# Optimization experiments

Measured on AMD Instinct MI355X. Metric: run time of the kernel, lower is better.

Reference implementation:

```python
import jax, jax.numpy as jnp
import numpy as np
import math

N, S, R = 1, 128, 256
CM, CZ, C, MSA_H, PAIR_H, CTM, FF = 256, 128, 32, 8, 4, 128, 4
SCALE = 1.0 / math.sqrt(C)


def _ln(x, w, b):
    m = jnp.mean(x, -1, keepdims=True)
    v = jnp.var(x, -1, keepdims=True)
    return (x - m) / jnp.sqrt(v + 1e-5) * w + b


def _gated_attn(x, gate_w, qkv_w, out_w, head, bias=None):
    # x: [n, s, r, cin]; attention over r within each (n, s, head)
    n, s, r, _ = x.shape
    gate = jax.nn.sigmoid(x @ gate_w).reshape(n, s, r, head, C)
    qkv = (x @ qkv_w).reshape(n, s, r, 3, head, C)
    q, k, v = qkv[..., 0, :, :], qkv[..., 1, :, :], qkv[..., 2, :, :]
    sim = jax.nn.softmax(jnp.einsum('nsqhc,nskhc->nshqk', q, k) * SCALE, axis=-1)
    if bias is not None:
        sim = sim + bias  # NOTE: source adds bias AFTER softmax; kept faithful
    att = jnp.einsum('nshqk,nskhc->nsqhc', sim, v) * gate
    return att.reshape(n, s, r, head * C) @ out_w


def _tri_mul(x, n1w, n1b, n2w, n2b, p1, p2, p3, p4, p5, p6, incoming):
    xn = _ln(x, n1w, n1b)
    a = jax.nn.sigmoid(xn @ p1) * (xn @ p2)
    b = jax.nn.sigmoid(xn @ p3) * (xn @ p4)
    if incoming:
        p = jnp.einsum('nrsk,nrtk->nstk', a, b)
        g = jnp.swapaxes(jax.nn.sigmoid(xn @ p6), 1, 2)
    else:
        p = jnp.einsum('nsrk,ntrk->nstk', a, b)
        g = jax.nn.sigmoid(xn @ p6)
    return (_ln(p, n2w, n2b) @ p5) * g


def setup_inputs() -> dict:
    keys = iter(jax.random.split(jax.random.key(0), 80))

    def rn(shape, scale=0.02):
        return jax.random.normal(next(keys), shape, dtype=jnp.float32) * scale

    ones = lambda n: jnp.ones((n,), jnp.float32)
    zeros = lambda n: jnp.zeros((n,), jnp.float32)
    d = dict(
        msa_repr=rn((N, S, R, CM), 1.0),
        pair_repr=rn((N, R, R, CZ), 1.0),
        row_norm_m_w=ones(CM), row_norm_m_b=zeros(CM),
        row_norm_z_w=ones(CZ), row_norm_z_b=zeros(CZ),
        row_gate=rn((CM, MSA_H * C)), row_qkv=rn((CM, 3 * MSA_H * C)),
        row_out=rn((MSA_H * C, CM)), row_bias=rn((CZ, MSA_H)),
        col_norm_w=ones(CM), col_norm_b=zeros(CM),
        col_gate=rn((CM, MSA_H * C)), col_qkv=rn((CM, 3 * MSA_H * C)),
        col_out=rn((MSA_H * C, CM)),
        mt_norm_w=ones(CM), mt_norm_b=zeros(CM),
        mt_p1=rn((CM, FF * CM)), mt_p2=rn((FF * CM, CM)),
        outer_norm_w=ones(CM), outer_norm_b=zeros(CM),
        outer_p1=rn((CM, C)), outer_p2=rn((CM, C)), outer_out=rn((C * C, CZ)),
        tmo_n1_w=ones(CZ), tmo_n1_b=zeros(CZ), tmo_n2_w=ones(CTM), tmo_n2_b=zeros(CTM),
        tmo_p1=rn((CZ, CTM)), tmo_p2=rn((CZ, CTM)), tmo_p3=rn((CZ, CTM)), tmo_p4=rn((CZ, CTM)),
        tmo_p5=rn((CTM, CZ)), tmo_p6=rn((CZ, CZ)),
        tmi_n1_w=ones(CZ), tmi_n1_b=zeros(CZ), tmi_n2_w=ones(CTM), tmi_n2_b=zeros(CTM),
        tmi_p1=rn((CZ, CTM)), tmi_p2=rn((CZ, CTM)), tmi_p3=rn((CZ, CTM)), tmi_p4=rn((CZ, CTM)),
        tmi_p5=rn((CTM, CZ)), tmi_p6=rn((CZ, CZ)),
        tas_norm_w=ones(CZ), tas_norm_b=zeros(CZ),
        tas_gate=rn((CZ, PAIR_H * C)), tas_qkv=rn((CZ, 3 * PAIR_H * C)),
        tas_out=rn((PAIR_H * C, CZ)), tas_bias=rn((CZ, PAIR_H)),
        tae_norm_w=ones(CZ), tae_norm_b=zeros(CZ),
        tae_gate=rn((CZ, PAIR_H * C)), tae_qkv=rn((CZ, 3 * PAIR_H * C)),
        tae_out=rn((PAIR_H * C, CZ)), tae_bias=rn((CZ, PAIR_H)),
        pt_norm_w=ones(CZ), pt_norm_b=zeros(CZ),
        pt_p1=rn((CZ, FF * CZ)), pt_p2=rn((FF * CZ, CZ)),
    )
    return d


def reference(msa_repr, pair_repr, row_norm_m_w, row_norm_m_b, row_norm_z_w, row_norm_z_b, row_gate, row_qkv, row_out, row_bias, col_norm_w, col_norm_b, col_gate, col_qkv, col_out, mt_norm_w, mt_norm_b, mt_p1, mt_p2, outer_norm_w, outer_norm_b, outer_p1, outer_p2, outer_out, tmo_n1_w, tmo_n1_b, tmo_n2_w, tmo_n2_b, tmo_p1, tmo_p2, tmo_p3, tmo_p4, tmo_p5, tmo_p6, tmi_n1_w, tmi_n1_b, tmi_n2_w, tmi_n2_b, tmi_p1, tmi_p2, tmi_p3, tmi_p4, tmi_p5, tmi_p6, tas_norm_w, tas_norm_b, tas_gate, tas_qkv, tas_out, tas_bias, tae_norm_w, tae_norm_b, tae_gate, tae_qkv, tae_out, tae_bias, pt_norm_w, pt_norm_b, pt_p1, pt_p2):
    msa, pair = msa_repr, pair_repr
    # 1. MSA row attention with pair bias
    xm = _ln(msa, row_norm_m_w, row_norm_m_b)
    xz = _ln(pair, row_norm_z_w, row_norm_z_b)
    bias = jnp.transpose(xz @ row_bias, (0, 3, 1, 2))[:, None]  # [N,1,H,R,R]
    msa = msa + _gated_attn(xm, row_gate, row_qkv, row_out, MSA_H, bias)
    # 2. MSA column attention
    xm = _ln(msa, col_norm_w, col_norm_b)
    msa = msa + jnp.swapaxes(_gated_attn(jnp.swapaxes(xm, 1, 2), col_gate, col_qkv, col_out, MSA_H), 1, 2)
    # 3. MSA transition
    xm = _ln(msa, mt_norm_w, mt_norm_b)
    msa = msa + jax.nn.relu(xm @ mt_p1) @ mt_p2
    # 4. outer product mean (no division in source; sum over s)
    xm = _ln(msa, outer_norm_w, outer_norm_b)
    a = jnp.swapaxes(xm @ outer_p1, 1, 2)  # [n,r,s,c]
    b = jnp.swapaxes(xm @ outer_p2, 1, 2)  # [n,t,s,c]
    outer = jnp.einsum('nrsc,ntse->nrtce', a, b).reshape(a.shape[0], a.shape[1], b.shape[1], C * C)
    pair = pair + outer @ outer_out
    # 5/6. triangle multiplicative updates (outgoing then incoming)
    pair = pair + _tri_mul(pair, tmo_n1_w, tmo_n1_b, tmo_n2_w, tmo_n2_b, tmo_p1, tmo_p2, tmo_p3, tmo_p4, tmo_p5, tmo_p6, False)
    pair = pair + _tri_mul(pair, tmi_n1_w, tmi_n1_b, tmi_n2_w, tmi_n2_b, tmi_p1, tmi_p2, tmi_p3, tmi_p4, tmi_p5, tmi_p6, True)
    # 7. triangle attention (node start)
    xz = _ln(pair, tas_norm_w, tas_norm_b)
    bias = jnp.transpose(xz @ tas_bias, (0, 1, 3, 2))[:, :, :, None, :]  # [N,S,H,1,R]
    pair = pair + _gated_attn(xz, tas_gate, tas_qkv, tas_out, PAIR_H, bias)
    # 8. triangle attention (node end): transpose residue axes
    xz = jnp.swapaxes(_ln(pair, tae_norm_w, tae_norm_b), 1, 2)
    bias = jnp.transpose(xz @ tae_bias, (0, 1, 3, 2))[:, :, :, None, :]
    pair = pair + jnp.swapaxes(_gated_attn(xz, tae_gate, tae_qkv, tae_out, PAIR_H, bias), 1, 2)
    # 9. pair transition
    xz = _ln(pair, pt_norm_w, pt_norm_b)
    pair = pair + jax.nn.relu(xz @ pt_p1) @ pt_p2
    return msa, pair
```

## Files before the change

### kernel.cpp

```cpp
#include <hip/hip_runtime.h>
#include <hip/hip_bf16.h>
#include <stdint.h>

typedef __hip_bfloat16 bf16;
typedef __attribute__((ext_vector_type(4))) int   i32x4;
typedef __attribute__((ext_vector_type(2))) unsigned u32x2;
typedef __attribute__((ext_vector_type(4))) float f32x4;


__device__ __forceinline__ float toF(float x){ return x; }
__device__ __forceinline__ float toF(bf16 x){ return __bfloat162float(x); }
__device__ __forceinline__ bf16  toB(float x){ return __float2bfloat16(x); }

__device__ __forceinline__ void gload16(const bf16* g, bf16* l){
    __builtin_amdgcn_global_load_lds((const __attribute__((address_space(1))) void*)g,
                                     (__attribute__((address_space(3))) void*)l, 16, 0, 0);
}

#define NW_IN 58
struct WStage {
    const void* src[NW_IN];
    int off[NW_IN];
    int K[NW_IN], N[NW_IN];
};
__global__ __launch_bounds__(256) void cvt_all_k(WStage t, bf16* __restrict__ base,
                                                 const uint32_t* __restrict__ probe){
    bool isbf = (probe[0] == 0x3F803F80u);
    const int wi = blockIdx.y;
    const void* in = t.src[wi];
    bf16* out = base + t.off[wi];
    const int K = t.K[wi], N = t.N[wi];
    const int total = K ? K*N : N;
    for (int i = blockIdx.x*256 + threadIdx.x; i < total; i += gridDim.x*256){
        float v = isbf ? toF(((const bf16*)in)[i]) : ((const float*)in)[i];
        if (K){ int k = i / N, n = i - k*N; out[(size_t)n*K + k] = toB(v); }
        else    out[i] = toB(v);
    }
}
__global__ void in2f_k(const void* __restrict__ in, float* __restrict__ out, int n,
                       const uint32_t* __restrict__ probe){
    bool isbf = (probe[0] == 0x3F803F80u);
    int i = blockIdx.x*256 + threadIdx.x;
    if (i < n) out[i] = isbf ? toF(((const bf16*)in)[i]) : ((const float*)in)[i];
}

template<typename T>
__global__ void ln_k(const T* __restrict__ x, const bf16* __restrict__ w, const bf16* __restrict__ b,
                     bf16* __restrict__ out, int D){
    int row = blockIdx.x, c = threadIdx.x;
    float v = toF(x[(size_t)row*D + c]);
    float s1 = v, s2 = v*v;
    #pragma unroll
    for (int o=32;o>0;o>>=1){ s1 += __shfl_down(s1,o); s2 += __shfl_down(s2,o); }
    __shared__ float r1[4], r2[4];
    int lane = c & 63, wid = c >> 6;
    if (lane==0){ r1[wid]=s1; r2[wid]=s2; }
    __syncthreads();
    int nw = blockDim.x >> 6;
    float m=0.f, q=0.f;
    for (int i=0;i<nw;i++){ m+=r1[i]; q+=r2[i]; }
    m /= (float)D; q = q/(float)D - m*m;
    float inv = rsqrtf(q + 1e-5f);
    out[(size_t)row*D + c] = toB((v-m)*inv*toF(w[c]) + toF(b[c]));
}

template<int MODE, int HN>
__global__ __launch_bounds__(256) void bproj_k(const bf16* __restrict__ xz, const bf16* __restrict__ Wb,
                                               bf16* __restrict__ outb){
    __shared__ float WbS[128*HN];
    const int i = blockIdx.x, t = threadIdx.x;
    for (int idx = t; idx < 128*HN; idx += 256) WbS[idx] = toF(Wb[idx]);
    __syncthreads();
    const bf16* row = xz + ((size_t)i*256 + t)*128;
    float d[HN] = {};
    #pragma unroll 4
    for (int c8 = 0; c8 < 16; ++c8){
        uint4 v = *(const uint4*)(row + c8*8);
        bf16 tmp[8]; *(uint4*)tmp = v;
        #pragma unroll
        for (int u=0;u<8;u++){
            float x = toF(tmp[u]);
            #pragma unroll
            for (int h=0;h<HN;h++) d[h] += x * WbS[(c8*8+u)*HN + h];
        }
    }
    #pragma unroll
    for (int h=0;h<HN;h++){
        size_t idx = (MODE==0) ? ((size_t)h*65536 + (size_t)i*256 + t)
                   : (MODE==1) ? ((size_t)(i*HN+h)*256 + t)
                               : ((size_t)(t*HN+h)*256 + i);
        outb[idx] = toB(d[h]);
    }
}

template<int ACT, int MUL, int RES, int HM>
__global__ __launch_bounds__(256) void mgemm_k(const bf16* __restrict__ A, const bf16* __restrict__ Bt,
                                               bf16* __restrict__ C, float* __restrict__ Res,
                                               const bf16* __restrict__ Mul,
                                               int M, int N, int K, int lda, size_t astep,
                                               int ldbt, size_t ldc, int res_off, int gtrans){
    __shared__ alignas(16) bf16 As[128*32];
    __shared__ alignas(16) bf16 Bs[128*32];
    const int tid  = threadIdx.x;
    const int m0   = blockIdx.y << 7, n0 = blockIdx.x << 7;
    const int lane = tid & 63, w = tid >> 6;
    const int wr   = (w >> 1) << 6, wc = (w & 1) << 6;
    const int fr   = lane & 15, fq = lane >> 4;
    const int sr = tid >> 2, sc = (tid & 3) << 3;
    const bf16* ga = A  + (size_t)(m0 + sr)*lda  + sc;
    const bf16* gb = Bt + (size_t)(n0 + sr)*ldbt + sc;
    bf16* la = As + tid*8;
    bf16* lb = Bs + tid*8;
    const size_t gaS = (size_t)64*lda, gbS = (size_t)64*ldbt;

    f32x4 acc[4][4] = {};
    for (int k0=0; k0<K; k0+=32){
        gload16(ga, la);        gload16(ga + gaS, la + 2048);
        gload16(gb, lb);        gload16(gb + gbS, lb + 2048);
        ga += astep; gb += 32;
        __syncthreads();
        i32x4 af[4], bv[4];
        #pragma unroll
        for (int i=0;i<4;i++) af[i] = *(const i32x4*)(As + ((wr + i*16 + fr) << 5) + (fq << 3));
        #pragma unroll
        for (int j=0;j<4;j++) bv[j] = *(const i32x4*)(Bs + ((wc + j*16 + fr) << 5) + (fq << 3));
        #pragma unroll
        for (int i=0;i<4;i++)
            #pragma unroll
            for (int j=0;j<4;j++)
                asm("v_mfma_f32_16x16x32_bf16 %0, %1, %2, %0"
                    : "+v"(acc[i][j]) : "v"(af[i]), "v"(bv[j]));
        __syncthreads();
    }
    #pragma unroll
    for (int i=0;i<4;i++){
        const int mB = m0 + wr + i*16 + (fq << 2);
        #pragma unroll
        for (int j=0;j<4;j++){
            const int n = n0 + wc + j*16 + fr;
            #pragma unroll
            for (int r=0;r<4;r++){
                int m = mB + r;
                float x = acc[i][j][r];
                if (ACT==1) x = 1.f/(1.f + __expf(-x));
                else if (ACT==2) x = fmaxf(x, 0.f);
                if (MUL){
                    int mr = gtrans ? (((m & 255) << 8) | (m >> 8)) : m;
                    x *= toF(Mul[(size_t)mr*N + n]);
                }
                if (RES) Res[(size_t)(m + res_off)*N + n] += x;
                else if (HM) C[(size_t)(n>>5)*ldc + (size_t)m*32 + (n&31)] = toB(x);
                else     C[(size_t)m*ldc + n] = toB(x);
            }
        }
    }
}

template<int ACT, int MUL, int RES, int GATE, int MHM>
__global__ __launch_bounds__(256) void sgemm_k(const bf16* __restrict__ A,
        const bf16* __restrict__ Bt1, const bf16* __restrict__ Bt2,
        bf16* __restrict__ C, float* __restrict__ Res, const bf16* __restrict__ Mul,
        int M, int lda, int ldbt, int ldc, size_t ldmul, int res_off, int gtrans){
    __shared__ alignas(16) bf16 Bs1[128*128];
    __shared__ alignas(16) bf16 Bs2[GATE ? 128*128 : 16];
    const int tid = threadIdx.x;
    for (int idx = tid; idx < 2048; idx += 256){
        int n = idx >> 4, cc = idx & 15;
        int sc = (cc ^ (n & 15)) << 3;
        *(uint4*)(Bs1 + n*128 + sc) = *(const uint4*)(Bt1 + (size_t)n*ldbt + (cc<<3));
        if (GATE)
            *(uint4*)(Bs2 + n*128 + sc) = *(const uint4*)(Bt2 + (size_t)n*ldbt + (cc<<3));
    }
    __syncthreads();
    const int lane = tid & 63, w = tid >> 6;
    const int fr = lane & 15, fq = lane >> 4;
    const int mb = blockIdx.x*128 + w*32;
    f32x4 acc[2][8] = {};
    f32x4 acc2[2][8] = {};
    #pragma unroll
    for (int k0=0;k0<4;k0++){
        i32x4 af[2];
        #pragma unroll
        for (int i=0;i<2;i++)
            af[i] = *(const i32x4*)(A + (size_t)(mb + i*16 + fr)*lda + k0*32 + fq*8);
        const int co = ((k0*4 + fq) ^ fr) << 3;
        #pragma unroll
        for (int j=0;j<8;j++){
            i32x4 bf1 = *(const i32x4*)(Bs1 + (j*16+fr)*128 + co);
            #pragma unroll
            for (int i=0;i<2;i++)
                asm("v_mfma_f32_16x16x32_bf16 %0, %1, %2, %0"
                    : "+v"(acc[i][j]) : "v"(af[i]), "v"(bf1));
            if (GATE){
                i32x4 bf2 = *(const i32x4*)(Bs2 + (j*16+fr)*128 + co);
                #pragma unroll
                for (int i=0;i<2;i++)
                    asm("v_mfma_f32_16x16x32_bf16 %0, %1, %2, %0"
                        : "+v"(acc2[i][j]) : "v"(af[i]), "v"(bf2));
            }
        }
    }
    #pragma unroll
    for (int i=0;i<2;i++){
        #pragma unroll
        for (int j=0;j<8;j++){
            const int n = j*16 + fr;
            #pragma unroll
            for (int r=0;r<4;r++){
                int m = mb + i*16 + (fq<<2) + r;
                float x = acc[i][j][r];
                if (GATE) x = acc2[i][j][r] / (1.f + __expf(-x));
                else if (ACT==1) x = 1.f/(1.f + __expf(-x));
                else if (ACT==2) x = fmaxf(x, 0.f);
                if (MUL){
                    int mr = gtrans ? (((m & 255) << 8) | (m >> 8)) : m;
                    if (MHM) x *= toF(Mul[(size_t)(n>>5)*ldmul + (size_t)mr*32 + (n&31)]);
                    else     x *= toF(Mul[(size_t)mr*ldmul + n]);
                }
                if (RES) Res[(size_t)(m + res_off)*128 + n] += x;
                else     C[(size_t)m*ldc + n] = toB(x);
            }
        }
    }
}

__global__ __launch_bounds__(256) void btrimul_k(const bf16* __restrict__ aT, const bf16* __restrict__ bT,
                                                 bf16* __restrict__ pT){
    __shared__ alignas(16) bf16 As[128*32];
    __shared__ alignas(16) bf16 Bs[128*32];
    const int tid  = threadIdx.x;
    const int m0   = blockIdx.y << 7, n0 = blockIdx.x << 7;
    const size_t zb = (size_t)blockIdx.z << 16;
    const int lane = tid & 63, w = tid >> 6;
    const int wr   = (w >> 1) << 6, wc = (w & 1) << 6;
    const int fr   = lane & 15, fq = lane >> 4;
    const int sr = tid >> 2, sc = (tid & 3) << 3;
    const bf16* ga = aT + zb + (size_t)(m0 + sr)*256 + sc;
    const bf16* gb = bT + zb + (size_t)(n0 + sr)*256 + sc;
    bf16* la = As + tid*8;
    bf16* lb = Bs + tid*8;
    const size_t gS = (size_t)64*256;

    f32x4 acc[4][4] = {};
    for (int k0=0; k0<256; k0+=32){
        gload16(ga, la);        gload16(ga + gS, la + 2048);
        gload16(gb, lb);        gload16(gb + gS, lb + 2048);
        ga += 32; gb += 32;
        __syncthreads();
        i32x4 af[4], bv[4];
        #pragma unroll
        for (int i=0;i<4;i++) af[i] = *(const i32x4*)(As + ((wr + i*16 + fr) << 5) + (fq << 3));
        #pragma unroll
        for (int j=0;j<4;j++) bv[j] = *(const i32x4*)(Bs + ((wc + j*16 + fr) << 5) + (fq << 3));
        #pragma unroll
        for (int i=0;i<4;i++)
            #pragma unroll
            for (int j=0;j<4;j++)
                asm("v_mfma_f32_16x16x32_bf16 %0, %1, %2, %0"
                    : "+v"(acc[i][j]) : "v"(af[i]), "v"(bv[j]));
        __syncthreads();
    }
    #pragma unroll
    for (int i=0;i<4;i++){
        const int mB = m0 + wr + i*16 + (fq << 2);
        #pragma unroll
        for (int j=0;j<4;j++){
            const int n = n0 + wc + j*16 + fr;
            #pragma unroll
            for (int r=0;r<4;r++)
                pT[zb + (size_t)(mB + r)*256 + n] = toB(acc[i][j][r]);
        }
    }
}

__global__ __launch_bounds__(256) void rc2k_k(const bf16* __restrict__ in, bf16* __restrict__ out, int swap){
    __shared__ uint16_t T[128][137];
    const int tt = blockIdx.x, tid = threadIdx.x;
    size_t base_pp, out_off; int ppstride;
    if (!swap){ base_pp = (size_t)tt*128;                  ppstride = 1;   out_off = (size_t)tt*128; }
    else      { int J = tt>>1, I0 = (tt&1)*128;
                base_pp = (size_t)I0*256 + J;              ppstride = 256; out_off = (size_t)J*256 + I0; }
    for (int it=0; it<8; ++it){
        int idx = tid + it*256;
        int r = idx >> 4, c8 = (idx & 15) << 3;
        uint4 v = *(const uint4*)(in + (base_pp + (size_t)r*ppstride)*128 + c8);
        uint16_t tmp[8]; *(uint4*)tmp = v;
        #pragma unroll
        for (int t=0;t<8;t++) T[r][c8+t] = tmp[t];
    }
    __syncthreads();
    for (int it=0; it<8; ++it){
        int idx = tid + it*256;
        int k = idx >> 4, r8 = (idx & 15) << 3;
        uint16_t tmp[8];
        #pragma unroll
        for (int t=0;t<8;t++) tmp[t] = T[r8+t][k];
        *(uint4*)(out + (size_t)k*65536 + out_off + r8) = *(uint4*)tmp;
    }
}
__global__ __launch_bounds__(256) void k2rc_k(const bf16* __restrict__ in, bf16* __restrict__ out){
    __shared__ uint16_t T[128][137];
    const int tt = blockIdx.x, tid = threadIdx.x;
    const size_t a0 = (size_t)tt*128;
    for (int it=0; it<8; ++it){
        int idx = tid + it*256;
        int k = idx >> 4, r8 = (idx & 15) << 3;
        uint4 v = *(const uint4*)(in + (size_t)k*65536 + a0 + r8);
        uint16_t tmp[8]; *(uint4*)tmp = v;
        #pragma unroll
        for (int t=0;t<8;t++) T[r8+t][k] = tmp[t];
    }
    __syncthreads();
    for (int it=0; it<8; ++it){
        int idx = tid + it*256;
        int r = idx >> 4, c8 = (idx & 15) << 3;
        uint16_t tmp[8];
        #pragma unroll
        for (int t=0;t<8;t++) tmp[t] = T[r][c8+t];
        *(uint4*)(out + (a0 + r)*128 + c8) = *(uint4*)tmp;
    }
}

template<int ACT, int MUL, int RES>
__global__ __launch_bounds__(256) void gemm_k(const bf16* __restrict__ A, const bf16* __restrict__ Bw,
                                              bf16* __restrict__ C, float* __restrict__ Res,
                                              const bf16* __restrict__ Mul,
                                              int M, int N, int K, int ldb, int res_off, int gtrans){
    __shared__ float As[64][33];
    __shared__ float Bs[32][65];
    int tid = threadIdx.x;
    int m0 = blockIdx.y*64, n0 = blockIdx.x*64;
    int tx = tid & 15, ty = tid >> 4;
    float acc[4][4] = {};
    for (int k0=0; k0<K; k0+=32){
        for (int i=tid; i<64*32; i+=256){
            int r = i>>5, cc = i&31;
            As[r][cc] = toF(A[(size_t)(m0+r)*K + k0 + cc]);
        }
        for (int i=tid; i<32*64; i+=256){
            int r = i>>6, cc = i&63; int col = n0+cc;
            Bs[r][cc] = (col < N) ? toF(Bw[(size_t)(k0+r)*ldb + col]) : 0.f;
        }
        __syncthreads();
        #pragma unroll 8
        for (int k=0;k<32;k++){
            float a4[4], b4[4];
            #pragma unroll
            for (int i=0;i<4;i++) a4[i] = As[ty*4+i][k];
            #pragma unroll
            for (int j=0;j<4;j++) b4[j] = Bs[k][tx*4+j];
            #pragma unroll
            for (int i=0;i<4;i++)
                #pragma unroll
                for (int j=0;j<4;j++) acc[i][j] += a4[i]*b4[j];
        }
        __syncthreads();
    }
    #pragma unroll
    for (int i=0;i<4;i++){
        int m = m0 + ty*4 + i;
        #pragma unroll
        for (int j=0;j<4;j++){
            int n = n0 + tx*4 + j;
            if (n >= N) continue;
            float x = acc[i][j];
            if (ACT==1) x = 1.f/(1.f + __expf(-x));
            else if (ACT==2) x = fmaxf(x, 0.f);
            if (MUL){
                int mr = gtrans ? (((m & 255) << 8) | (m >> 8)) : m;
                x *= toF(Mul[(size_t)mr*N + n]);
            }
            if (RES) Res[(size_t)(m + res_off)*N + n] += x;
            else     C[(size_t)m*N + n] = toB(x);
        }
    }
}

template<int BIAS, int L>
__global__ __launch_bounds__(256) void attn4_k(bf16* __restrict__ QO,
                                               const bf16* __restrict__ Kp, const bf16* __restrict__ Vp,
                                               const bf16* __restrict__ bias,
                                               int H, size_t HS, int sO, int sL){
    constexpr int MW  = L/4;
    constexpr int IFR = MW/16;
    constexpr int KC  = 32;
    constexpr int NCH = L/KC;
    constexpr int VP  = L + 8;
    constexpr int PTW = 44;
    __shared__ alignas(16) bf16 K_lds[L*40];
    __shared__ alignas(16) bf16 VT_lds[32*VP];
    __shared__ alignas(16) bf16 PT_lds[4*MW*PTW];
    __shared__ float red[8*32 + 32];
    const int o = blockIdx.y, h = blockIdx.x, tid = threadIdx.x;
    const int lane = tid & 63, w = tid >> 6;
    const int fr = lane & 15, fq = lane >> 4;
    const size_t hb = (size_t)h*HS;

    for (int idx = tid; idx < L*4; idx += 256){
        int l = idx >> 2, c8 = (idx & 3) << 3;
        size_t p = hb + (size_t)(o*sO + l*sL)*32 + c8;
        *(uint4*)(K_lds + l*40 + c8) = *(const uint4*)(Kp + p);
        uint4 vv = *(const uint4*)(Vp + p);
        bf16 tmp[8]; *(uint4*)tmp = vv;
        #pragma unroll
        for (int t=0;t<8;t++) VT_lds[(c8+t)*VP + l] = tmp[t];
    }
    __syncthreads();

    float* ObS = red + 256;
    if (BIAS == 2){
        int c = tid & 31, g = tid >> 5;
        const bf16* bp = bias + (size_t)(o*H + h)*256;
        float p = 0.f;
        for (int k = g*(L/8); k < (g+1)*(L/8); ++k)
            p += toF(bp[k]) * toF(VT_lds[c*VP + k]);
        red[g*32 + c] = p;
        __syncthreads();
        if (tid < 32){
            float s = 0.f;
            #pragma unroll
            for (int g2=0; g2<8; ++g2) s += red[g2*32 + tid];
            ObS[tid] = s;
        }
        __syncthreads();
    }

    i32x4 qf[IFR];
    #pragma unroll
    for (int i=0;i<IFR;i++){
        int q = w*MW + i*16 + fr;
        qf[i] = *(const i32x4*)(QO + hb + (size_t)(o*sO + q*sL)*32 + fq*8);
    }
    bf16* Pw = PT_lds + w*MW*PTW;
    f32x4 accO[IFR][2] = {};
    f32x4 accB[IFR][2] = {};
    float ls[IFR] = {};

    for (int ch=0; ch<NCH; ++ch){
        const int k0 = ch*KC;
        f32x4 sa[IFR][2] = {};
        i32x4 kf[2];
        #pragma unroll
        for (int j=0;j<2;j++) kf[j] = *(const i32x4*)(K_lds + (k0 + j*16 + fr)*40 + fq*8);
        #pragma unroll
        for (int i=0;i<IFR;i++)
            #pragma unroll
            for (int j=0;j<2;j++)
                asm("v_mfma_f32_16x16x32_bf16 %0, %1, %2, %0"
                    : "+v"(sa[i][j]) : "v"(kf[j]), "v"(qf[i]));
        #pragma unroll
        for (int i=0;i<IFR;i++){
            #pragma unroll
            for (int j=0;j<2;j++){
                float e0 = __expf(sa[i][j][0] * 0.17677669529663687f);
                float e1 = __expf(sa[i][j][1] * 0.17677669529663687f);
                float e2 = __expf(sa[i][j][2] * 0.17677669529663687f);
                float e3 = __expf(sa[i][j][3] * 0.17677669529663687f);
                ls[i] += (e0+e1) + (e2+e3);
                unsigned d0, d1;
                asm("v_cvt_pk_bf16_f32 %0, %1, %2" : "=v"(d0) : "v"(e0), "v"(e1));
                asm("v_cvt_pk_bf16_f32 %0, %1, %2" : "=v"(d1) : "v"(e2), "v"(e3));
                u32x2 dd = {d0, d1};
                *(u32x2*)(Pw + (i*16 + fr)*PTW + j*16 + fq*4) = dd;
            }
        }
        i32x4 vf[2];
        #pragma unroll
        for (int j=0;j<2;j++) vf[j] = *(const i32x4*)(VT_lds + (j*16 + fr)*VP + k0 + fq*8);
        #pragma unroll
        for (int i=0;i<IFR;i++){
            i32x4 pa = *(const i32x4*)(Pw + (i*16 + fr)*PTW + fq*8);
            #pragma unroll
            for (int j=0;j<2;j++)
                asm("v_mfma_f32_16x16x32_bf16 %0, %1, %2, %0"
                    : "+v"(accO[i][j]) : "v"(pa), "v"(vf[j]));
        }
        if (BIAS == 1){
            #pragma unroll
            for (int i=0;i<IFR;i++){
                i32x4 ba = *(const i32x4*)(bias + (size_t)h*65536
                               + (size_t)(w*MW + i*16 + fr)*256 + k0 + fq*8);
                #pragma unroll
                for (int j=0;j<2;j++)
                    asm("v_mfma_f32_16x16x32_bf16 %0, %1, %2, %0"
                        : "+v"(accB[i][j]) : "v"(ba), "v"(vf[j]));
            }
        }
    }
    #pragma unroll
    for (int i=0;i<IFR;i++){
        float s = ls[i];
        s += __shfl_xor(s, 16); s += __shfl_xor(s, 32);
        ls[i] = 1.f / s;
    }
    #pragma unroll
    for (int i=0;i<IFR;i++)
        #pragma unroll
        for (int j=0;j<2;j++)
            #pragma unroll
            for (int r=0;r<4;r++){
                int q = w*MW + i*16 + fq*4 + r;
                int c = j*16 + fr;
                float inv = __shfl(ls[i], fq*4 + r);
                float v = accO[i][j][r]*inv;
                if (BIAS==1) v += accB[i][j][r];
                if (BIAS==2) v += ObS[c];
                QO[hb + (size_t)(o*sO + q*sL)*32 + c] = toB(v);
            }
}

__global__ void mulsigHM_k(bf16* __restrict__ a, const bf16* __restrict__ g, size_t HS, int NC, int n){
    int i = blockIdx.x*256 + threadIdx.x;
    if (i < n){
        int m = i / NC, col = i - m*NC;
        int h = col >> 5, c = col & 31;
        size_t o = (size_t)h*HS + (size_t)m*32 + c;
        float sg = 1.f/(1.f + __expf(-toF(g[(size_t)m*NC + col])));
        a[o] = toB(toF(a[o]) * sg);
    }
}

__global__ __launch_bounds__(256) void outer_k(const bf16* __restrict__ ap, const bf16* __restrict__ bp,
                                               bf16* __restrict__ outc, int r0){
    int t = blockIdx.x, rl = blockIdx.y, r = r0 + rl;
    __shared__ float As[128*32], Bs[128*32];
    for (int idx=threadIdx.x; idx<128*32; idx+=256){
        int s = idx>>5, c = idx&31;
        As[idx] = toF(ap[((size_t)s*256 + r)*32 + c]);
        Bs[idx] = toF(bp[((size_t)s*256 + t)*32 + c]);
    }
    __syncthreads();
    int ce0 = threadIdx.x*4;
    int c = ce0 >> 5, e0 = ce0 & 31;
    float acc[4] = {0.f,0.f,0.f,0.f};
    for (int s=0;s<128;s++){
        float av = As[s*32 + c];
        #pragma unroll
        for (int j=0;j<4;j++) acc[j] += av*Bs[s*32 + e0 + j];
    }
    size_t row = (size_t)rl*256 + t;
    #pragma unroll
    for (int j=0;j<4;j++) outc[row*1024 + ce0 + j] = toB(acc[j]);
}

static bool tshape(int i, int& K, int& N){
    switch(i){
        case 6: case 8: case 12: case 14: K=256; N=256;  return true;
        case 7: case 13:                  K=256; N=768;  return true;
        case 17:                          K=256; N=1024; return true;
        case 18:                          K=1024;N=256;  return true;
        case 23:                          K=1024;N=128;  return true;
        case 47: case 53:                 K=128; N=384;  return true;
        case 58:                          K=128; N=512;  return true;
        case 59:                          K=512; N=128;  return true;
        default:
            if ((i>=28&&i<=33)||(i>=38&&i<=43)||i==46||i==48||i==52||i==54){ K=128; N=128; return true; }
            return false;
    }
}

extern "C" void kernel_launch(void* const* d_in, const int* in_sizes, int n_in,
                              void* d_out, int out_size, void* d_ws, size_t ws_size,
                              hipStream_t stream){
    (void)n_in; (void)out_size; (void)ws_size;
    const int MSA_N  = 128*256*256;
    const int PAIR_N = 256*256*128;
    const size_t HSm = (size_t)32768*32;
    const size_t HSp = (size_t)65536*32;
    const uint32_t* probe = (const uint32_t*)d_in[2];

    char*  w     = (char*)d_ws;
    bf16*  wsts  = (bf16*)(w);
    bf16*  biasB = (bf16*)(w + 4194304);
    bf16*  lnb   = (bf16*)(w + 6291456);
    bf16*  bufA  = (bf16*)(w + 23068672);
    bf16*  bufB  = (bf16*)(w + 39845888);
    bf16*  bufC  = (bf16*)(w + 56623104);

    float* msaF  = (float*)d_out;
    float* pairF = msaF + MSA_N;

    size_t woff[64]; { size_t acc = 0;
        for (int i=2;i<60;i++){ woff[i] = acc; acc += ((size_t)in_sizes[i] + 63) & ~(size_t)63; } }
    #define W(i) (wsts + woff[i])

    {
        WStage st;
        for (int i=2;i<60;i++){
            int tk, tn;
            st.src[i-2] = d_in[i];
            st.off[i-2] = (int)woff[i];
            if (tshape(i, tk, tn)){ st.K[i-2]=tk; st.N[i-2]=tn; }
            else                   { st.K[i-2]=0;  st.N[i-2]=in_sizes[i]; }
        }
        cvt_all_k<<<dim3(64, NW_IN),256,0,stream>>>(st, wsts, probe);
    }

    in2f_k<<<32768,256,0,stream>>>(d_in[0], msaF,  MSA_N,  probe);
    in2f_k<<<32768,256,0,stream>>>(d_in[1], pairF, PAIR_N, probe);

    ln_k<float><<<32768,256,0,stream>>>(msaF, W(2), W(3), lnb, 256);
    ln_k<float><<<65536,128,0,stream>>>(pairF, W(4), W(5), bufC, 128);
    bproj_k<0,8><<<256,256,0,stream>>>(bufC, W(9), biasB);
    mgemm_k<0,0,0,1><<<dim3(6,256),256,0,stream>>>(lnb, W(7), bufA, nullptr, nullptr,
                                                   32768,768,256, 256,32,256, HSm, 0,0);
    attn4_k<1,256><<<dim3(8,128),256,0,stream>>>(bufA, bufA+8*HSm, bufA+16*HSm, biasB, 8, HSm, 256, 1);
    mgemm_k<0,0,0,0><<<dim3(2,256),256,0,stream>>>(lnb, W(6), bufA+8*HSm, nullptr, nullptr,
                                                   32768,256,256, 256,32,256, 256, 0,0);
    mulsigHM_k<<<32768,256,0,stream>>>(bufA, bufA+8*HSm, HSm, 256, MSA_N);
    mgemm_k<0,0,1,0><<<dim3(2,256),256,0,stream>>>(bufA, W(8), nullptr, msaF, nullptr,
                                                   32768,256,256, 32,HSm,256, 256, 0,0);

    ln_k<float><<<32768,256,0,stream>>>(msaF, W(10), W(11), lnb, 256);
    mgemm_k<0,0,0,1><<<dim3(6,256),256,0,stream>>>(lnb, W(13), bufA, nullptr, nullptr,
                                                   32768,768,256, 256,32,256, HSm, 0,0);
    attn4_k<0,128><<<dim3(8,256),256,0,stream>>>(bufA, bufA+8*HSm, bufA+16*HSm, nullptr, 8, HSm, 1, 256);
    mgemm_k<0,0,0,0><<<dim3(2,256),256,0,stream>>>(lnb, W(12), bufA+8*HSm, nullptr, nullptr,
                                                   32768,256,256, 256,32,256, 256, 0,0);
    mulsigHM_k<<<32768,256,0,stream>>>(bufA, bufA+8*HSm, HSm, 256, MSA_N);
    mgemm_k<0,0,1,0><<<dim3(2,256),256,0,stream>>>(bufA, W(14), nullptr, msaF, nullptr,
                                                   32768,256,256, 32,HSm,256, 256, 0,0);

    ln_k<float><<<32768,256,0,stream>>>(msaF, W(15), W(16), lnb, 256);
    for (int ch=0; ch<4; ++ch){
        mgemm_k<2,0,0,0><<<dim3(2,256),256,0,stream>>>(lnb, W(17)+ch*65536, bufA, nullptr, nullptr,
                                                       32768,256,256, 256,32,256, 256, 0,0);
        mgemm_k<0,0,1,0><<<dim3(2,256),256,0,stream>>>(bufA, W(18)+ch*256, nullptr, msaF, nullptr,
                                                       32768,256,256, 256,32,1024, 256, 0,0);
    }

    ln_k<float><<<32768,256,0,stream>>>(msaF, W(19), W(20), lnb, 256);
    gemm_k<0,0,0><<<dim3(1,512),256,0,stream>>>(lnb, W(21), bufA, nullptr, nullptr, 32768,32,256, 32, 0,0);
    gemm_k<0,0,0><<<dim3(1,512),256,0,stream>>>(lnb, W(22), bufB, nullptr, nullptr, 32768,32,256, 32, 0,0);
    for (int ch=0; ch<8; ++ch){
        outer_k<<<dim3(256,32),256,0,stream>>>(bufA, bufB, lnb, ch*32);
        mgemm_k<0,0,1,0><<<dim3(1,64),256,0,stream>>>(lnb, W(23), nullptr, pairF, nullptr,
                                                      8192,128,1024, 1024,32,1024, 128, ch*8192,0);
    }

    for (int tm=0; tm<2; ++tm){
        int o = tm ? 34 : 24;
        int inc = tm;
        ln_k<float><<<65536,128,0,stream>>>(pairF, W(o+0), W(o+1), lnb, 128);
        sgemm_k<0,0,0,1,0><<<512,256,0,stream>>>(lnb, W(o+4), W(o+5), bufA, nullptr, nullptr,
                                                 65536, 128,128,128,0, 0,0);
        sgemm_k<0,0,0,1,0><<<512,256,0,stream>>>(lnb, W(o+6), W(o+7), bufB, nullptr, nullptr,
                                                 65536, 128,128,128,0, 0,0);
        rc2k_k<<<512,256,0,stream>>>(bufA, bufC, inc);
        rc2k_k<<<512,256,0,stream>>>(bufB, bufA, inc);
        btrimul_k<<<dim3(2,2,128),256,0,stream>>>(bufC, bufA, bufB);
        k2rc_k<<<512,256,0,stream>>>(bufB, bufC);
        ln_k<bf16><<<65536,128,0,stream>>>(bufC, W(o+2), W(o+3), bufC, 128);
        sgemm_k<1,0,0,0,0><<<512,256,0,stream>>>(lnb, W(o+9), nullptr, bufA, nullptr, nullptr,
                                                 65536, 128,128,128,0, 0,0);
        sgemm_k<0,1,1,0,0><<<512,256,0,stream>>>(bufC, W(o+8), nullptr, nullptr, pairF, bufA,
                                                 65536, 128,128,0,128, 0, inc);
    }

    ln_k<float><<<65536,128,0,stream>>>(pairF, W(44), W(45), lnb, 128);
    bproj_k<1,4><<<256,256,0,stream>>>(lnb, W(49), biasB);
    mgemm_k<0,0,0,1><<<dim3(3,512),256,0,stream>>>(lnb, W(47), bufA, nullptr, nullptr,
                                                   65536,384,128, 128,32,128, HSp, 0,0);
    attn4_k<2,256><<<dim3(4,256),256,0,stream>>>(bufA, bufA+4*HSp, bufA+8*HSp, biasB, 4, HSp, 256, 1);
    sgemm_k<1,1,0,0,1><<<512,256,0,stream>>>(lnb, W(46), nullptr, bufA+4*HSp, nullptr, bufA,
                                             65536, 128,128,128, HSp, 0,0);
    sgemm_k<0,0,1,0,0><<<512,256,0,stream>>>(bufA+4*HSp, W(48), nullptr, nullptr, pairF, nullptr,
                                             65536, 128,128,0,0, 0,0);
    ln_k<float><<<65536,128,0,stream>>>(pairF, W(50), W(51), lnb, 128);
    bproj_k<2,4><<<256,256,0,stream>>>(lnb, W(55), biasB);
    mgemm_k<0,0,0,1><<<dim3(3,512),256,0,stream>>>(lnb, W(53), bufA, nullptr, nullptr,
                                                   65536,384,128, 128,32,128, HSp, 0,0);
    attn4_k<2,256><<<dim3(4,256),256,0,stream>>>(bufA, bufA+4*HSp, bufA+8*HSp, biasB, 4, HSp, 1, 256);
    sgemm_k<1,1,0,0,1><<<512,256,0,stream>>>(lnb, W(52), nullptr, bufA+4*HSp, nullptr, bufA,
                                             65536, 128,128,128, HSp, 0,0);
    sgemm_k<0,0,1,0,0><<<512,256,0,stream>>>(bufA+4*HSp, W(54), nullptr, nullptr, pairF, nullptr,
                                             65536, 128,128,0,0, 0,0);

    ln_k<float><<<65536,128,0,stream>>>(pairF, W(56), W(57), lnb, 128);
    for (int ch=0; ch<4; ++ch){
        sgemm_k<2,0,0,0,0><<<512,256,0,stream>>>(lnb, W(58)+ch*16384, nullptr, bufA, nullptr, nullptr,
                                                 65536, 128,128,128,0, 0,0);
        sgemm_k<0,0,1,0,0><<<512,256,0,stream>>>(bufA, W(59)+ch*128, nullptr, nullptr, pairF, nullptr,
                                                 65536, 128,512,0,0, 0,0);
    }
}
```

Before: 2.412 ms.

## Compute outer-product-mean via transposed inputs and MFMA GEMM instead of scalar kernel

Replaces the scalar FP32 shared-memory outer_k kernel with a transpose of the a/b projections into [r,c,s] layout, followed by the existing MFMA-based mgemm_k. A new HM==2 store mode scatters the GEMM output straight into the [r,t,c*e] layout that the following projection GEMM consumes. The aim is to move the outer-product-mean contraction onto matrix cores. The cost is two extra transpose kernels and a scattered output write pattern.

Measured after the change: 2.062 ms. 14.5% less time.

```diff
diff --git a/kernel.cpp b/kernel.cpp
--- a/kernel.cpp
+++ b/kernel.cpp
@@ -149,7 +149,9 @@
                     x *= toF(Mul[(size_t)mr*N + n]);
                 }
                 if (RES) Res[(size_t)(m + res_off)*N + n] += x;
-                else if (HM) C[(size_t)(n>>5)*ldc + (size_t)m*32 + (n&31)] = toB(x);
+                else if (HM==1) C[(size_t)(n>>5)*ldc + (size_t)m*32 + (n&31)] = toB(x);
+                else if (HM==2) C[((size_t)(m>>5)*256 + (size_t)(n>>5))*ldc
+                                  + (size_t)(m&31)*32 + (n&31)] = toB(x);
                 else     C[(size_t)m*ldc + n] = toB(x);
             }
         }
@@ -318,6 +320,30 @@
         #pragma unroll
         for (int t=0;t<8;t++) tmp[t] = T[r][c8+t];
         *(uint4*)(out + (a0 + r)*128 + c8) = *(uint4*)tmp;
+    }
+}
+
+__global__ __launch_bounds__(256) void t32_k(const bf16* __restrict__ in, bf16* __restrict__ out){
+    __shared__ uint16_t T[128][36];
+    const int r = blockIdx.x, tid = threadIdx.x;
+    #pragma unroll
+    for (int it=0; it<2; ++it){
+        int idx = tid + it*256;
+        int s = idx >> 2, u = idx & 3;
+        uint4 v = *(const uint4*)(in + ((size_t)(s*256 + r))*32 + u*8);
+        uint16_t tmp[8]; *(uint4*)tmp = v;
+        #pragma unroll
+        for (int t=0;t<8;t++) T[s][u*8+t] = tmp[t];
+    }
+    __syncthreads();
+    #pragma unroll
+    for (int it=0; it<2; ++it){
+        int idx = tid + it*256;
+        int c = idx >> 4, s8 = (idx & 15) << 3;
+        uint16_t tmp[8];
+        #pragma unroll
+        for (int t=0;t<8;t++) tmp[t] = T[s8+t][c];
+        *(uint4*)(out + ((size_t)(r*32 + c))*128 + s8) = *(uint4*)tmp;
     }
 }
 
@@ -520,29 +546,6 @@
     }
 }
 
-__global__ __launch_bounds__(256) void outer_k(const bf16* __restrict__ ap, const bf16* __restrict__ bp,
-                                               bf16* __restrict__ outc, int r0){
-    int t = blockIdx.x, rl = blockIdx.y, r = r0 + rl;
-    __shared__ float As[128*32], Bs[128*32];
-    for (int idx=threadIdx.x; idx<128*32; idx+=256){
-        int s = idx>>5, c = idx&31;
-        As[idx] = toF(ap[((size_t)s*256 + r)*32 + c]);
-        Bs[idx] = toF(bp[((size_t)s*256 + t)*32 + c]);
-    }
-    __syncthreads();
-    int ce0 = threadIdx.x*4;
-    int c = ce0 >> 5, e0 = ce0 & 31;
-    float acc[4] = {0.f,0.f,0.f,0.f};
-    for (int s=0;s<128;s++){
-        float av = As[s*32 + c];
-        #pragma unroll
-        for (int j=0;j<4;j++) acc[j] += av*Bs[s*32 + e0 + j];
-    }
-    size_t row = (size_t)rl*256 + t;
-    #pragma unroll
-    for (int j=0;j<4;j++) outc[row*1024 + ce0 + j] = toB(acc[j]);
-}
-
 static bool tshape(int i, int& K, int& N){
     switch(i){
         case 6: case 8: case 12: case 14: K=256; N=256;  return true;
@@ -632,10 +635,17 @@
     ln_k<float><<<32768,256,0,stream>>>(msaF, W(19), W(20), lnb, 256);
     gemm_k<0,0,0><<<dim3(1,512),256,0,stream>>>(lnb, W(21), bufA, nullptr, nullptr, 32768,32,256, 32, 0,0);
     gemm_k<0,0,0><<<dim3(1,512),256,0,stream>>>(lnb, W(22), bufB, nullptr, nullptr, 32768,32,256, 32, 0,0);
-    for (int ch=0; ch<8; ++ch){
-        outer_k<<<dim3(256,32),256,0,stream>>>(bufA, bufB, lnb, ch*32);
-        mgemm_k<0,0,1,0><<<dim3(1,64),256,0,stream>>>(lnb, W(23), nullptr, pairF, nullptr,
-                                                      8192,128,1024, 1024,32,1024, 128, ch*8192,0);
+    {
+        bf16* aT = bufC;
+        bf16* bT = bufC + 1048576;
+        t32_k<<<256,256,0,stream>>>(bufA, aT);
+        t32_k<<<256,256,0,stream>>>(bufB, bT);
+        for (int ch=0; ch<8; ++ch){
+            mgemm_k<0,0,0,2><<<dim3(64,8),256,0,stream>>>(aT + (size_t)ch*131072, bT, lnb, nullptr, nullptr,
+                                                          1024,8192,128, 128,32,128, 1024, 0,0);
+            mgemm_k<0,0,1,0><<<dim3(1,64),256,0,stream>>>(lnb, W(23), nullptr, pairF, nullptr,
+                                                          8192,128,1024, 1024,32,1024, 128, ch*8192,0);
+        }
     }
 
     for (int tm=0; tm<2; ++tm){
```
